# Optimization experiments

Hardware: AMD Instinct MI355X
Metric: run time of the kernel (lower is better)

Reference implementation:

```python
import jax, jax.numpy as jnp
import numpy as np

# Llama-3-8B-like attention, prefill over B sequences of length S (flattened tokens)
D = 4096      # hidden_size
N = 32        # num query heads
K = 8         # num KV heads (GQA)
H = 128       # head_dim (== head_dim_original, already a multiple of 128 so no padding)
B = 4         # sequences in the ragged batch
S = 1024      # tokens per sequence
T = B * S     # total flattened tokens
ROPE_THETA = 10000.0


def _apply_rope(x, positions, head_dim, theta):
    # x: [T, n_heads, H]; positions: [T] int
    inv_freq = 1.0 / (theta ** (jnp.arange(0, head_dim, 2, dtype=jnp.float32) / head_dim))
    freqs = positions.astype(jnp.float32)[:, None] * inv_freq[None, :]  # [T, H/2]
    emb = jnp.concatenate([freqs, freqs], axis=-1)                       # [T, H]
    cos = jnp.cos(emb)[:, None, :].astype(x.dtype)
    sin = jnp.sin(emb)[:, None, :].astype(x.dtype)
    x1, x2 = jnp.split(x, 2, axis=-1)
    rotated = jnp.concatenate([-x2, x1], axis=-1)
    return x * cos + rotated * sin


def setup_inputs() -> dict:
    key = jax.random.key(0)
    ks = jax.random.split(key, 5)
    x = jax.random.normal(ks[0], (T, D), dtype=jnp.float32)
    # positions restart per sequence (ragged prefill metadata)
    input_positions = (jnp.arange(T, dtype=jnp.int32) % S)
    w_scale = 0.02
    Wq = jax.random.normal(ks[1], (D, N, H), dtype=jnp.float32) * w_scale
    Wk = jax.random.normal(ks[2], (D, K, H), dtype=jnp.float32) * w_scale
    Wv = jax.random.normal(ks[3], (D, K, H), dtype=jnp.float32) * w_scale
    Wo = jax.random.normal(ks[4], (N, H, D), dtype=jnp.float32) * w_scale
    return {"x": x, "input_positions": input_positions,
            "Wq": Wq, "Wk": Wk, "Wv": Wv, "Wo": Wo}


def reference(x, input_positions, Wq, Wk, Wv, Wo):
    # QKV projections (flattened tokens)
    q = jnp.einsum('td,dnh->tnh', x, Wq)   # [T, N, H]
    k = jnp.einsum('td,dkh->tkh', x, Wk)   # [T, K, H]
    v = jnp.einsum('td,dkh->tkh', x, Wv)   # [T, K, H]
    q = _apply_rope(q, input_positions, H, ROPE_THETA)
    k = _apply_rope(k, input_positions, H, ROPE_THETA)

    # Ragged causal attention: per-sequence causal SDPA with GQA head grouping.
    G = N // K  # query heads per KV head
    qb = q.reshape(B, S, K, G, H)
    kb = k.reshape(B, S, K, H)
    vb = v.reshape(B, S, K, H)
    scale = jnp.asarray(H, q.dtype) ** -0.5  # head_dim_original ** -0.5
    scores = jnp.einsum('bqkgh,bskh->bkgqs', qb, kb) * scale  # [B,K,G,S,S]
    causal = jnp.tril(jnp.ones((S, S), dtype=bool))
    scores = jnp.where(causal, scores, jnp.finfo(scores.dtype).min)
    probs = jax.nn.softmax(scores, axis=-1)
    out = jnp.einsum('bkgqs,bskh->bqkgh', probs, vb).reshape(T, N, H)

    # Output projection
    o = jnp.einsum('tnh,nhd->td', out, Wo)  # [T, D]
    return o
```

## Files before the change

kernel.cpp:

```cpp
#include <hip/hip_runtime.h>
#include <cstdint>


typedef unsigned short u16;
typedef short bf16x8 __attribute__((ext_vector_type(8)));
typedef float f32x4 __attribute__((ext_vector_type(4)));

#define L2E 1.44269504088896340736f

static __device__ __forceinline__ u16 f2bf(float f) {
  union { float f; unsigned u; } v; v.f = f;
  unsigned r = (v.u + 0x7fffu + ((v.u >> 16) & 1u)) >> 16;
  return (u16)r;
}
static __device__ __forceinline__ float bf2f(u16 h) {
  union { unsigned u; float f; } v; v.u = ((unsigned)h) << 16;
  return v.f;
}

typedef __attribute__((address_space(1))) const unsigned int gas_u32;
typedef __attribute__((address_space(3))) unsigned int las_u32;
static __device__ __forceinline__ void glds16(const void* g, const void* l) {
  __builtin_amdgcn_global_load_lds((gas_u32*)(uintptr_t)g,
                                   (las_u32*)(unsigned)(uintptr_t)l, 16, 0, 0);
}

__global__ __launch_bounds__(256) void cvt_kernel(const float4* __restrict__ in,
                                                  uint2* __restrict__ out, int n4) {
  int i = blockIdx.x * 256 + threadIdx.x;
  if (i < n4) {
    float4 v = in[i];
    uint2 r;
    r.x = (unsigned)f2bf(v.x) | ((unsigned)f2bf(v.y) << 16);
    r.y = (unsigned)f2bf(v.z) | ((unsigned)f2bf(v.w) << 16);
    out[i] = r;
  }
}

__global__ __launch_bounds__(256) void tcvt_kernel(const float* __restrict__ in,
                                                   u16* __restrict__ out, int R, int C) {
  __shared__ float tile[32][33];
  int tx = threadIdx.x, ty = threadIdx.y;
  int r0 = blockIdx.y * 32, c0 = blockIdx.x * 32;
#pragma unroll
  for (int j = 0; j < 4; ++j)
    tile[ty + j * 8][tx] = in[(size_t)(r0 + ty + j * 8) * C + c0 + tx];
  __syncthreads();
#pragma unroll
  for (int j = 0; j < 4; ++j)
    out[(size_t)(c0 + ty + j * 8) * R + r0 + tx] = f2bf(tile[tx][ty + j * 8]);
}

template <int BF16OUT>
__global__ __launch_bounds__(512, 2) void gemm_nt8(const u16* __restrict__ A,
                                                   const u16* __restrict__ Bm,
                                                   void* __restrict__ Cp,
                                                   int M, int N, int Kd) {
  __shared__ u16 Als[2][2][8192];
  __shared__ u16 Bls[2][2][8192];
  const int tid = threadIdx.x;
  const int w = tid >> 6, lane = tid & 63;
  const int ln15 = lane & 15, quad = lane >> 4;
  const int wm = w & 1, wn = w >> 1;

  const int nbm = M >> 8;
  const int nwg = nbm * (N >> 8);
  const int cpx = nwg >> 3;
  const int bid = blockIdx.x;
  const int swz = (bid & 7) * cpx + (bid >> 3);
  const int bm = swz & (nbm - 1);
  const int bn = swz / nbm;
  const int m0 = bm << 8, n0 = bn << 8;

  const int nt = Kd >> 6;

  const int srow = lane >> 2;
  const int schk = ((lane & 3) ^ ((lane >> 3) & 3)) << 3;
  const u16* aSrc = A + (size_t)(m0 + w * 32 + srow) * Kd + schk;
  const u16* bSrc = Bm + (size_t)(n0 + w * 32 + srow) * Kd + schk;
  const int ldsb = w * 1024;

  const int rswz = (quad ^ ((ln15 >> 1) & 3)) << 3;
  const int aoff = (wm * 128 + ln15) * 32 + rswz;
  const int boff = (wn * 64 + ln15) * 32 + rswz;
  const unsigned aAddr = (unsigned)(uintptr_t)&Als[0][0][aoff];
  const unsigned bAddr = (unsigned)(uintptr_t)&Bls[0][0][boff];

  f32x4 acc[8][4];
#pragma unroll
  for (int i = 0; i < 8; ++i)
#pragma unroll
    for (int j = 0; j < 4; ++j) acc[i][j] = f32x4{0.f, 0.f, 0.f, 0.f};
  bf16x8 af[8];

#define DSR(dst, addr, off) \
  asm volatile("ds_read_b128 %0, %1 offset:%2" : "=v"(dst) : "v"(addr), "i"(off))

#define STA(kt, buf, ks)                                          \
  do {                                                            \
    int kc_ = (kt) < nt ? (kt) : nt - 1;                          \
    const u16* s_ = aSrc + (size_t)kc_ * 64 + (ks) * 32;          \
    glds16(s_, &Als[buf][ks][ldsb]);                              \
    glds16(s_ + (size_t)16 * Kd, &Als[buf][ks][ldsb + 512]);      \
  } while (0)
#define STB(kt, buf, ks)                                          \
  do {                                                            \
    int kc_ = (kt) < nt ? (kt) : nt - 1;                          \
    const u16* s_ = bSrc + (size_t)kc_ * 64 + (ks) * 32;          \
    glds16(s_, &Bls[buf][ks][ldsb]);                              \
    glds16(s_ + (size_t)16 * Kd, &Bls[buf][ks][ldsb + 512]);      \
  } while (0)

#define PHASE(buf, ks, nh, STAGE, VM)                                              \
  do {                                                                             \
    if ((nh) == 0) {                                                               \
      DSR(af[0], aAddr, (buf)*32768 + (ks)*16384 + 0 * 1024);                      \
      DSR(af[1], aAddr, (buf)*32768 + (ks)*16384 + 1 * 1024);                      \
      DSR(af[2], aAddr, (buf)*32768 + (ks)*16384 + 2 * 1024);                      \
      DSR(af[3], aAddr, (buf)*32768 + (ks)*16384 + 3 * 1024);                      \
      DSR(af[4], aAddr, (buf)*32768 + (ks)*16384 + 4 * 1024);                      \
      DSR(af[5], aAddr, (buf)*32768 + (ks)*16384 + 5 * 1024);                      \
      DSR(af[6], aAddr, (buf)*32768 + (ks)*16384 + 6 * 1024);                      \
      DSR(af[7], aAddr, (buf)*32768 + (ks)*16384 + 7 * 1024);                      \
    }                                                                              \
    bf16x8 b0_, b1_;                                                               \
    DSR(b0_, bAddr, (buf)*32768 + (ks)*16384 + (nh)*2048);                         \
    DSR(b1_, bAddr, (buf)*32768 + (ks)*16384 + (nh)*2048 + 1024);                  \
    STAGE;                                                                         \
    __builtin_amdgcn_s_barrier();                                                  \
    asm volatile("s_waitcnt lgkmcnt(0)" ::: "memory");                             \
    __builtin_amdgcn_sched_barrier(0);                                             \
    __builtin_amdgcn_s_setprio(1);                                                 \
    _Pragma("unroll") for (int m_ = 0; m_ < 8; ++m_) {                             \
      acc[m_][2 * (nh)] =                                                          \
          __builtin_amdgcn_mfma_f32_16x16x32_bf16(af[m_], b0_, acc[m_][2 * (nh)],  \
                                                  0, 0, 0);                        \
      acc[m_][2 * (nh) + 1] = __builtin_amdgcn_mfma_f32_16x16x32_bf16(             \
          af[m_], b1_, acc[m_][2 * (nh) + 1], 0, 0, 0);                            \
    }                                                                              \
    __builtin_amdgcn_s_setprio(0);                                                 \
    if (VM) asm volatile("s_waitcnt vmcnt(6)" ::: "memory");                       \
    __builtin_amdgcn_s_barrier();                                                  \
    __builtin_amdgcn_sched_barrier(0);                                             \
  } while (0)

  STA(0, 0, 0); STB(0, 0, 0); STA(0, 0, 1); STB(0, 0, 1);
  STA(1, 1, 0); STB(1, 1, 0); STA(1, 1, 1);
  asm volatile("s_waitcnt vmcnt(6)" ::: "memory");
  __builtin_amdgcn_s_barrier();
  __builtin_amdgcn_sched_barrier(0);

  const int iters = nt >> 1;
  for (int i = 0; i < iters; ++i) {
    const int t = 2 * i;
    PHASE(0, 0, 0, STB(t + 1, 1, 1), 0);
    PHASE(0, 0, 1, STA(t + 2, 0, 0), 0);
    PHASE(0, 1, 0, STB(t + 2, 0, 0), 0);
    PHASE(0, 1, 1, STA(t + 2, 0, 1), 1);
    PHASE(1, 0, 0, STB(t + 2, 0, 1), 0);
    PHASE(1, 0, 1, STA(t + 3, 1, 0), 0);
    PHASE(1, 1, 0, STB(t + 3, 1, 0), 0);
    PHASE(1, 1, 1, STA(t + 3, 1, 1), 1);
  }
#undef PHASE
#undef STA
#undef STB
#undef DSR

  const int crow = m0 + wm * 128 + quad * 4;
  const int ccol = n0 + wn * 64 + ln15;
#pragma unroll
  for (int m = 0; m < 8; ++m)
#pragma unroll
    for (int j = 0; j < 4; ++j)
#pragma unroll
      for (int r = 0; r < 4; ++r) {
        float v = acc[m][j][r];
        if (BF16OUT)
          ((u16*)Cp)[(size_t)(crow + m * 16 + r) * N + ccol + j * 16] = f2bf(v);
        else
          ((float*)Cp)[(size_t)(crow + m * 16 + r) * N + ccol + j * 16] = v;
      }
}

__global__ __launch_bounds__(256) void ropetab_kernel(float2* __restrict__ tab) {
  int idx = blockIdx.x * 256 + threadIdx.x;
  int i = idx & 63;
  float inv = exp2f(-0.20751874963942190927f * (float)i);
  float f = (float)(idx >> 6) * inv;
  float s, c;
  sincosf(f, &s, &c);
  tab[idx] = make_float2(c, s);
}

__global__ __launch_bounds__(256) void rope_kernel(u16* __restrict__ qkv,
                                                   const int* __restrict__ pos,
                                                   const float2* __restrict__ tab,
                                                   int total) {
  int idx = blockIdx.x * 256 + threadIdx.x;
  if (idx >= total) return;
  int t = idx / 2560;
  int rem = idx - t * 2560;
  int head = rem >> 6;
  int i = rem & 63;
  float2 cs = tab[(pos[t] << 6) | i];
  float c = cs.x, s = cs.y;
  int colbase = (head < 32) ? head * 128 : (4096 + (head - 32) * 128);
  u16* base = qkv + (size_t)t * 6144 + colbase;
  float x1 = bf2f(base[i]), x2 = bf2f(base[i + 64]);
  float o1 = x1 * c - x2 * s;
  float o2 = x2 * c + x1 * s;
  if (head < 32) { o1 *= 0.08838834764831845f; o2 *= 0.08838834764831845f; }
  base[i] = f2bf(o1);
  base[i + 64] = f2bf(o2);
}

__global__ __launch_bounds__(256, 3) void attn_kernel(const u16* __restrict__ qkv,
                                                      u16* __restrict__ outp) {
  __shared__ u16 Klds[64 * 128];
  __shared__ u16 Vtlds[128 * 72];
  __shared__ u16 Plds[4 * 16 * 72];

  const int bx = blockIdx.x;
  const int qb = 15 - (bx & 15);
  const int n = (bx >> 4) & 31;
  const int b = bx >> 9;
  const int kh = n >> 2;

  const int tid = threadIdx.x;
  const int w = tid >> 6;
  const int lane = tid & 63;
  const int ln15 = lane & 15;
  const int quad = lane >> 4;

  const int ldq = 6144;
  const int seq0 = b << 10;
  const int q0 = seq0 + qb * 64;

  const u16* Qg = qkv + n * 128;
  const u16* Kg = qkv + 4096 + kh * 128;
  const u16* Vg = qkv + 5120 + kh * 128;

  bf16x8 qf[4];
  {
    const u16* qrow = Qg + (size_t)(q0 + w * 16 + ln15) * ldq + quad * 8;
#pragma unroll
    for (int ks = 0; ks < 4; ++ks) qf[ks] = *(const bf16x8*)(qrow + ks * 32);
  }

  f32x4 o[8];
#pragma unroll
  for (int i = 0; i < 8; ++i) o[i] = f32x4{0.f, 0.f, 0.f, 0.f};
  float m_r[4] = {-INFINITY, -INFINITY, -INFINITY, -INFINITY};
  float l_r[4] = {0.f, 0.f, 0.f, 0.f};

  const int krow = w * 4 + (lane >> 4);
  const int kcol = (((lane & 15) ^ (krow & 7)) << 3);

  const int vs0 = (lane & 31) * 2;
  const int vhb = w * 32 + (lane >> 5) * 16;

  union V16 { uint4 v[2]; u16 s[16]; };
  V16 ra, rb;
  {
    const u16* v0 = Vg + (size_t)(seq0 + vs0) * ldq + vhb;
    ra.v[0] = *(const uint4*)v0;
    ra.v[1] = *(const uint4*)(v0 + 8);
    rb.v[0] = *(const uint4*)(v0 + ldq);
    rb.v[1] = *(const uint4*)(v0 + ldq + 8);
  }

  for (int kt = 0; kt <= qb; ++kt) {
    __syncthreads();
    {
      const u16* kbase = Kg + (size_t)(seq0 + kt * 64 + krow) * ldq + kcol;
#pragma unroll
      for (int q = 0; q < 4; ++q)
        glds16(kbase + (size_t)q * 16 * ldq, &Klds[(q * 16 + w * 4) * 128]);
    }
    {
#pragma unroll
      for (int j = 0; j < 16; ++j) {
        unsigned pk = (unsigned)ra.s[j] | ((unsigned)rb.s[j] << 16);
        *(unsigned*)&Vtlds[(vhb + j) * 72 + vs0] = pk;
      }
    }
    __syncthreads();

    if (kt < qb) {
      const u16* v0 = Vg + (size_t)(seq0 + (kt + 1) * 64 + vs0) * ldq + vhb;
      ra.v[0] = *(const uint4*)v0;
      ra.v[1] = *(const uint4*)(v0 + 8);
      rb.v[0] = *(const uint4*)(v0 + ldq);
      rb.v[1] = *(const uint4*)(v0 + ldq + 8);
    }

    f32x4 sfr[4];
#pragma unroll
    for (int c = 0; c < 4; ++c) {
      f32x4 acc = f32x4{0.f, 0.f, 0.f, 0.f};
#pragma unroll
      for (int ks = 0; ks < 4; ++ks) {
        int rr = c * 16 + ln15;
        int ph = (ks * 4 + quad) ^ (rr & 7);
        bf16x8 kf = *(const bf16x8*)&Klds[rr * 128 + ph * 8];
        acc = __builtin_amdgcn_mfma_f32_16x16x32_bf16(qf[ks], kf, acc, 0, 0, 0);
      }
      sfr[c] = acc;
    }

    if (kt == qb) {
#pragma unroll
      for (int c = 0; c < 4; ++c) {
        int col = c * 16 + ln15;
#pragma unroll
        for (int r = 0; r < 4; ++r)
          if (col > w * 16 + quad * 4 + r) sfr[c][r] = -INFINITY;
      }
    }

    float mx[4];
#pragma unroll
    for (int r = 0; r < 4; ++r) {
      float m0 = fmaxf(fmaxf(sfr[0][r], sfr[1][r]), fmaxf(sfr[2][r], sfr[3][r]));
      m0 = fmaxf(m0, __shfl_xor(m0, 1));
      m0 = fmaxf(m0, __shfl_xor(m0, 2));
      m0 = fmaxf(m0, __shfl_xor(m0, 4));
      m0 = fmaxf(m0, __shfl_xor(m0, 8));
      mx[r] = m0;
    }
    float ex = fmaxf(fmaxf(mx[0] - m_r[0], mx[1] - m_r[1]),
                     fmaxf(mx[2] - m_r[2], mx[3] - m_r[3]));
    if (!__all(ex <= 8.f)) {
#pragma unroll
      for (int r = 0; r < 4; ++r) {
        float mnew = fmaxf(m_r[r], mx[r]);
        float al = exp2f((m_r[r] - mnew) * L2E);
        m_r[r] = mnew;
        l_r[r] *= al;
#pragma unroll
        for (int ht = 0; ht < 8; ++ht) o[ht][r] *= al;
      }
    }
#pragma unroll
    for (int r = 0; r < 4; ++r) {
      float rs = 0.f;
#pragma unroll
      for (int c = 0; c < 4; ++c) {
        float pv = exp2f((sfr[c][r] - m_r[r]) * L2E);
        sfr[c][r] = pv;
        rs += pv;
      }
      rs += __shfl_xor(rs, 1);
      rs += __shfl_xor(rs, 2);
      rs += __shfl_xor(rs, 4);
      rs += __shfl_xor(rs, 8);
      l_r[r] += rs;
    }

#pragma unroll
    for (int c = 0; c < 4; ++c)
#pragma unroll
      for (int r = 0; r < 4; ++r)
        Plds[w * 1152 + (quad * 4 + r) * 72 + c * 16 + ln15] = f2bf(sfr[c][r]);

    asm volatile("s_waitcnt lgkmcnt(0)" ::: "memory");

    bf16x8 pf[2];
#pragma unroll
    for (int ks = 0; ks < 2; ++ks)
      pf[ks] = *(const bf16x8*)&Plds[w * 1152 + ln15 * 72 + ks * 32 + quad * 8];
#pragma unroll
    for (int ht = 0; ht < 8; ++ht) {
#pragma unroll
      for (int ks = 0; ks < 2; ++ks) {
        bf16x8 vf = *(const bf16x8*)&Vtlds[(ht * 16 + ln15) * 72 + ks * 32 + quad * 8];
        o[ht] = __builtin_amdgcn_mfma_f32_16x16x32_bf16(pf[ks], vf, o[ht], 0, 0, 0);
      }
    }
  }

#pragma unroll
  for (int r = 0; r < 4; ++r) l_r[r] = 1.f / l_r[r];
#pragma unroll
  for (int ht = 0; ht < 8; ++ht)
#pragma unroll
    for (int r = 0; r < 4; ++r)
      outp[(size_t)(q0 + w * 16 + quad * 4 + r) * 4096 + n * 128 + ht * 16 + ln15] =
          f2bf(o[ht][r] * l_r[r]);
}

extern "C" void kernel_launch(void* const* d_in, const int* in_sizes, int n_in,
                              void* d_out, int out_size, void* d_ws, size_t ws_size,
                              hipStream_t stream) {
  const float* x = (const float*)d_in[0];
  const int* posi = (const int*)d_in[1];
  const float* Wq = (const float*)d_in[2];
  const float* Wk = (const float*)d_in[3];
  const float* Wv = (const float*)d_in[4];
  const float* Wo = (const float*)d_in[5];
  float* out = (float*)d_out;
  char* ws = (char*)d_ws;

  u16* xb = (u16*)(ws);
  u16* Wt = (u16*)(ws + 33554432);
  u16* WoT = (u16*)(ws + 83886080);
  u16* qkv = (u16*)(ws + 117440512);
  u16* attn = xb;
  float2* rtab = (float2*)ws;

  cvt_kernel<<<16384, 256, 0, stream>>>((const float4*)x, (uint2*)xb, 4194304);
  tcvt_kernel<<<dim3(128, 128), dim3(32, 8), 0, stream>>>(Wq, Wt, 4096, 4096);
  tcvt_kernel<<<dim3(32, 128), dim3(32, 8), 0, stream>>>(Wk, Wt + (size_t)4096 * 4096, 4096, 1024);
  tcvt_kernel<<<dim3(32, 128), dim3(32, 8), 0, stream>>>(Wv, Wt + (size_t)5120 * 4096, 4096, 1024);
  tcvt_kernel<<<dim3(128, 128), dim3(32, 8), 0, stream>>>(Wo, WoT, 4096, 4096);

  gemm_nt8<1><<<dim3(384), 512, 0, stream>>>(xb, Wt, qkv, 4096, 6144, 4096);
  ropetab_kernel<<<256, 256, 0, stream>>>(rtab);
  rope_kernel<<<40960, 256, 0, stream>>>(qkv, posi, rtab, 10485760);
  attn_kernel<<<2048, 256, 0, stream>>>(qkv, attn);
  gemm_nt8<0><<<dim3(256), 512, 0, stream>>>(attn, WoT, out, 4096, 4096, 4096);
}
```

Before: 750.3 us.

## Share K/V tiles across GQA head group and double-buffer K loads

```diff
diff --git a/kernel.cpp b/kernel.cpp
--- a/kernel.cpp
+++ b/kernel.cpp
@@ -215,23 +215,25 @@
   base[i + 64] = f2bf(o2);
 }
 
-__global__ __launch_bounds__(256, 3) void attn_kernel(const u16* __restrict__ qkv,
+__global__ __launch_bounds__(512, 2) void attn_kernel(const u16* __restrict__ qkv,
                                                       u16* __restrict__ outp) {
-  __shared__ u16 Klds[64 * 128];
+  __shared__ u16 Klds[2][64 * 128];
   __shared__ u16 Vtlds[128 * 72];
-  __shared__ u16 Plds[4 * 16 * 72];
+  __shared__ u16 Plds[8 * 32 * 72];
 
   const int bx = blockIdx.x;
-  const int qb = 15 - (bx & 15);
-  const int n = (bx >> 4) & 31;
-  const int b = bx >> 9;
-  const int kh = n >> 2;
+  const int qb = 15 - (bx >> 5);
+  const int kh = bx & 7;
+  const int b = (bx >> 3) & 3;
 
   const int tid = threadIdx.x;
   const int w = tid >> 6;
   const int lane = tid & 63;
   const int ln15 = lane & 15;
   const int quad = lane >> 4;
+  const int g = w & 3;
+  const int half = w >> 2;
+  const int n = kh * 4 + g;
 
   const int ldq = 6144;
   const int seq0 = b << 10;
@@ -241,46 +243,49 @@
   const u16* Kg = qkv + 4096 + kh * 128;
   const u16* Vg = qkv + 5120 + kh * 128;
 
-  bf16x8 qf[4];
-  {
-    const u16* qrow = Qg + (size_t)(q0 + w * 16 + ln15) * ldq + quad * 8;
-#pragma unroll
-    for (int ks = 0; ks < 4; ++ks) qf[ks] = *(const bf16x8*)(qrow + ks * 32);
+  bf16x8 qf[2][4];
+#pragma unroll
+  for (int rf = 0; rf < 2; ++rf) {
+    const u16* qrow = Qg + (size_t)(q0 + half * 32 + rf * 16 + ln15) * ldq + quad * 8;
+#pragma unroll
+    for (int ks = 0; ks < 4; ++ks) qf[rf][ks] = *(const bf16x8*)(qrow + ks * 32);
   }
 
-  f32x4 o[8];
-#pragma unroll
-  for (int i = 0; i < 8; ++i) o[i] = f32x4{0.f, 0.f, 0.f, 0.f};
-  float m_r[4] = {-INFINITY, -INFINITY, -INFINITY, -INFINITY};
-  float l_r[4] = {0.f, 0.f, 0.f, 0.f};
-
-  const int krow = w * 4 + (lane >> 4);
-  const int kcol = (((lane & 15) ^ (krow & 7)) << 3);
-
-  const int vs0 = (lane & 31) * 2;
-  const int vhb = w * 32 + (lane >> 5) * 16;
-
-  union V16 { uint4 v[2]; u16 s[16]; };
-  V16 ra, rb;
+  f32x4 o[2][8];
+#pragma unroll
+  for (int rf = 0; rf < 2; ++rf)
+#pragma unroll
+    for (int i = 0; i < 8; ++i) o[rf][i] = f32x4{0.f, 0.f, 0.f, 0.f};
+  float m_r[2][4], l_r[2][4];
+#pragma unroll
+  for (int rf = 0; rf < 2; ++rf)
+#pragma unroll
+    for (int r = 0; r < 4; ++r) { m_r[rf][r] = -INFINITY; l_r[rf][r] = 0.f; }
+
+  const int kr0 = w * 8 + (lane >> 4);
+  const int kr1 = kr0 + 4;
+  const u16* kp0 = Kg + (size_t)(seq0 + kr0) * ldq + (((lane & 15) ^ (kr0 & 7)) << 3);
+  const u16* kp1 = Kg + (size_t)(seq0 + kr1) * ldq + (((lane & 15) ^ (kr1 & 7)) << 3);
+
+  const int vs0 = (tid & 31) * 2;
+  const int vhb = (tid >> 5) * 8;
+
+  union V8 { uint4 v; u16 s[8]; };
+  V8 ra, rb;
   {
     const u16* v0 = Vg + (size_t)(seq0 + vs0) * ldq + vhb;
-    ra.v[0] = *(const uint4*)v0;
-    ra.v[1] = *(const uint4*)(v0 + 8);
-    rb.v[0] = *(const uint4*)(v0 + ldq);
-    rb.v[1] = *(const uint4*)(v0 + ldq + 8);
+    ra.v = *(const uint4*)v0;
+    rb.v = *(const uint4*)(v0 + ldq);
+    glds16(kp0, &Klds[0][(w * 8) * 128]);
+    glds16(kp1, &Klds[0][(w * 8 + 4) * 128]);
   }
 
   for (int kt = 0; kt <= qb; ++kt) {
+    const int cur = kt & 1;
     __syncthreads();
     {
-      const u16* kbase = Kg + (size_t)(seq0 + kt * 64 + krow) * ldq + kcol;
-#pragma unroll
-      for (int q = 0; q < 4; ++q)
-        glds16(kbase + (size_t)q * 16 * ldq, &Klds[(q * 16 + w * 4) * 128]);
-    }
-    {
-#pragma unroll
-      for (int j = 0; j < 16; ++j) {
+#pragma unroll
+      for (int j = 0; j < 8; ++j) {
         unsigned pk = (unsigned)ra.s[j] | ((unsigned)rb.s[j] << 16);
         *(unsigned*)&Vtlds[(vhb + j) * 72 + vs0] = pk;
       }
@@ -288,106 +293,132 @@
     __syncthreads();
 
     if (kt < qb) {
+      glds16(kp0 + (size_t)(kt + 1) * 64 * ldq, &Klds[cur ^ 1][(w * 8) * 128]);
+      glds16(kp1 + (size_t)(kt + 1) * 64 * ldq, &Klds[cur ^ 1][(w * 8 + 4) * 128]);
       const u16* v0 = Vg + (size_t)(seq0 + (kt + 1) * 64 + vs0) * ldq + vhb;
-      ra.v[0] = *(const uint4*)v0;
-      ra.v[1] = *(const uint4*)(v0 + 8);
-      rb.v[0] = *(const uint4*)(v0 + ldq);
-      rb.v[1] = *(const uint4*)(v0 + ldq + 8);
+      ra.v = *(const uint4*)v0;
+      rb.v = *(const uint4*)(v0 + ldq);
     }
 
-    f32x4 sfr[4];
-#pragma unroll
-    for (int c = 0; c < 4; ++c) {
-      f32x4 acc = f32x4{0.f, 0.f, 0.f, 0.f};
-#pragma unroll
-      for (int ks = 0; ks < 4; ++ks) {
-        int rr = c * 16 + ln15;
-        int ph = (ks * 4 + quad) ^ (rr & 7);
-        bf16x8 kf = *(const bf16x8*)&Klds[rr * 128 + ph * 8];
-        acc = __builtin_amdgcn_mfma_f32_16x16x32_bf16(qf[ks], kf, acc, 0, 0, 0);
-      }
-      sfr[c] = acc;
+    f32x4 sfr[2][4];
+#pragma unroll
+    for (int rf = 0; rf < 2; ++rf)
+#pragma unroll
+      for (int c = 0; c < 4; ++c) {
+        f32x4 acc = f32x4{0.f, 0.f, 0.f, 0.f};
+#pragma unroll
+        for (int ks = 0; ks < 4; ++ks) {
+          int rr = c * 16 + ln15;
+          int ph = (ks * 4 + quad) ^ (rr & 7);
+          bf16x8 kf = *(const bf16x8*)&Klds[cur][rr * 128 + ph * 8];
+          acc = __builtin_amdgcn_mfma_f32_16x16x32_bf16(qf[rf][ks], kf, acc, 0, 0, 0);
+        }
+        sfr[rf][c] = acc;
+      }
+
+    if (kt == qb) {
+#pragma unroll
+      for (int rf = 0; rf < 2; ++rf)
+#pragma unroll
+        for (int c = 0; c < 4; ++c) {
+          int col = c * 16 + ln15;
+#pragma unroll
+          for (int r = 0; r < 4; ++r)
+            if (col > half * 32 + rf * 16 + quad * 4 + r) sfr[rf][c][r] = -INFINITY;
+        }
     }
 
-    if (kt == qb) {
-#pragma unroll
-      for (int c = 0; c < 4; ++c) {
-        int col = c * 16 + ln15;
+    float mx[2][4];
+#pragma unroll
+    for (int rf = 0; rf < 2; ++rf)
+#pragma unroll
+      for (int r = 0; r < 4; ++r) {
+        float m0 = fmaxf(fmaxf(sfr[rf][0][r], sfr[rf][1][r]),
+                         fmaxf(sfr[rf][2][r], sfr[rf][3][r]));
+        m0 = fmaxf(m0, __shfl_xor(m0, 1));
+        m0 = fmaxf(m0, __shfl_xor(m0, 2));
+        m0 = fmaxf(m0, __shfl_xor(m0, 4));
+        m0 = fmaxf(m0, __shfl_xor(m0, 8));
+        mx[rf][r] = m0;
+      }
+    float ex = -INFINITY;
+#pragma unroll
+    for (int rf = 0; rf < 2; ++rf)
+#pragma unroll
+      for (int r = 0; r < 4; ++r) ex = fmaxf(ex, mx[rf][r] - m_r[rf][r]);
+    if (!__all(ex <= 8.f)) {
+#pragma unroll
+      for (int rf = 0; rf < 2; ++rf)
+#pragma unroll
+        for (int r = 0; r < 4; ++r) {
+          float mnew = fmaxf(m_r[rf][r], mx[rf][r]);
+          float al = exp2f((m_r[rf][r] - mnew) * L2E);
+          m_r[rf][r] = mnew;
+          l_r[rf][r] *= al;
+#pragma unroll
+          for (int ht = 0; ht < 8; ++ht) o[rf][ht][r] *= al;
+        }
+    }
+#pragma unroll
+    for (int rf = 0; rf < 2; ++rf)
+#pragma unroll
+      for (int r = 0; r < 4; ++r) {
+        float rs = 0.f;
+#pragma unroll
+        for (int c = 0; c < 4; ++c) {
+          float pv = exp2f((sfr[rf][c][r] - m_r[rf][r]) * L2E);
+          sfr[rf][c][r] = pv;
+          rs += pv;
+        }
+        rs += __shfl_xor(rs, 1);
+        rs += __shfl_xor(rs, 2);
+        rs += __shfl_xor(rs, 4);
+        rs += __shfl_xor(rs, 8);
+        l_r[rf][r] += rs;
+      }
+
+#pragma unroll
+    for (int rf = 0; rf < 2; ++rf)
+#pragma unroll
+      for (int c = 0; c < 4; ++c)
 #pragma unroll
         for (int r = 0; r < 4; ++r)
-          if (col > w * 16 + quad * 4 + r) sfr[c][r] = -INFINITY;
-      }
-    }
-
-    float mx[4];
-#pragma unroll
-    for (int r = 0; r < 4; ++r) {
-      float m0 = fmaxf(fmaxf(sfr[0][r], sfr[1][r]), fmaxf(sfr[2][r], sfr[3][r]));
-      m0 = fmaxf(m0, __shfl_xor(m0, 1));
-      m0 = fmaxf(m0, __shfl_xor(m0, 2));
-      m0 = fmaxf(m0, __shfl_xor(m0, 4));
-      m0 = fmaxf(m0, __shfl_xor(m0, 8));
-      mx[r] = m0;
-    }
-    float ex = fmaxf(fmaxf(mx[0] - m_r[0], mx[1] - m_r[1]),
-                     fmaxf(mx[2] - m_r[2], mx[3] - m_r[3]));
-    if (!__all(ex <= 8.f)) {
-#pragma unroll
-      for (int r = 0; r < 4; ++r) {
-        float mnew = fmaxf(m_r[r], mx[r]);
-        float al = exp2f((m_r[r] - mnew) * L2E);
-        m_r[r] = mnew;
-        l_r[r] *= al;
-#pragma unroll
-        for (int ht = 0; ht < 8; ++ht) o[ht][r] *= al;
-      }
-    }
-#pragma unroll
-    for (int r = 0; r < 4; ++r) {
-      float rs = 0.f;
-#pragma unroll
-      for (int c = 0; c < 4; ++c) {
-        float pv = exp2f((sfr[c][r] - m_r[r]) * L2E);
-        sfr[c][r] = pv;
-        rs += pv;
-      }
-      rs += __shfl_xor(rs, 1);
-      rs += __shfl_xor(rs, 2);
-      rs += __shfl_xor(rs, 4);
-      rs += __shfl_xor(rs, 8);
-      l_r[r] += rs;
-    }
-
-#pragma unroll
-    for (int c = 0; c < 4; ++c)
-#pragma unroll
-      for (int r = 0; r < 4; ++r)
-        Plds[w * 1152 + (quad * 4 + r) * 72 + c * 16 + ln15] = f2bf(sfr[c][r]);
+          Plds[w * 2304 + (rf * 16 + quad * 4 + r) * 72 + c * 16 + ln15] =
+              f2bf(sfr[rf][c][r]);
 
     asm volatile("s_waitcnt lgkmcnt(0)" ::: "memory");
 
-    bf16x8 pf[2];
-#pragma unroll
-    for (int ks = 0; ks < 2; ++ks)
-      pf[ks] = *(const bf16x8*)&Plds[w * 1152 + ln15 * 72 + ks * 32 + quad * 8];
-#pragma unroll
-    for (int ht = 0; ht < 8; ++ht) {
+    bf16x8 pf[2][2];
+#pragma unroll
+    for (int rf = 0; rf < 2; ++rf)
+#pragma unroll
+      for (int ks = 0; ks < 2; ++ks)
+        pf[rf][ks] =
+            *(const bf16x8*)&Plds[w * 2304 + (rf * 16 + ln15) * 72 + ks * 32 + quad * 8];
+#pragma unroll
+    for (int ht = 0; ht < 8; ++ht)
 #pragma unroll
       for (int ks = 0; ks < 2; ++ks) {
         bf16x8 vf = *(const bf16x8*)&Vtlds[(ht * 16 + ln15) * 72 + ks * 32 + quad * 8];
-        o[ht] = __builtin_amdgcn_mfma_f32_16x16x32_bf16(pf[ks], vf, o[ht], 0, 0, 0);
-      }
-    }
+#pragma unroll
+        for (int rf = 0; rf < 2; ++rf)
+          o[rf][ht] = __builtin_amdgcn_mfma_f32_16x16x32_bf16(pf[rf][ks], vf, o[rf][ht],
+                                                              0, 0, 0);
+      }
   }
 
 #pragma unroll
-  for (int r = 0; r < 4; ++r) l_r[r] = 1.f / l_r[r];
-#pragma unroll
-  for (int ht = 0; ht < 8; ++ht)
-#pragma unroll
-    for (int r = 0; r < 4; ++r)
-      outp[(size_t)(q0 + w * 16 + quad * 4 + r) * 4096 + n * 128 + ht * 16 + ln15] =
-          f2bf(o[ht][r] * l_r[r]);
+  for (int rf = 0; rf < 2; ++rf)
+#pragma unroll
+    for (int r = 0; r < 4; ++r) l_r[rf][r] = 1.f / l_r[rf][r];
+#pragma unroll
+  for (int rf = 0; rf < 2; ++rf)
+#pragma unroll
+    for (int ht = 0; ht < 8; ++ht)
+#pragma unroll
+      for (int r = 0; r < 4; ++r)
+        outp[(size_t)(q0 + half * 32 + rf * 16 + quad * 4 + r) * 4096 + n * 128 +
+             ht * 16 + ln15] = f2bf(o[rf][ht][r] * l_r[rf][r]);
 }
 
 extern "C" void kernel_launch(void* const* d_in, const int* in_sizes, int n_in,
@@ -418,6 +449,6 @@
   gemm_nt8<1><<<dim3(384), 512, 0, stream>>>(xb, Wt, qkv, 4096, 6144, 4096);
   ropetab_kernel<<<256, 256, 0, stream>>>(rtab);
   rope_kernel<<<40960, 256, 0, stream>>>(qkv, posi, rtab, 10485760);
-  attn_kernel<<<2048, 256, 0, stream>>>(qkv, attn);
+  attn_kernel<<<512, 512, 0, stream>>>(qkv, attn);
   gemm_nt8<0><<<dim3(256), 512, 0, stream>>>(attn, WoT, out, 4096, 4096, 4096);
 }
```

Measured after the change: 687.6 us. 8.4% less time.
